# Optimization experiments

Measured on AMD Instinct MI355X. Metric: run time of the kernel, lower is better.

The kernel has to match this reference:

```python
import jax, jax.numpy as jnp
import numpy as np

SEQ, D, H, FF = 2048, 1024, 16, 4096
HD = D // H  # head_dim = 64


def setup_inputs() -> dict:
    key = jax.random.key(0)
    ks = jax.random.split(key, 13)
    s = lambda k, shape, fan_in: jax.random.normal(k, shape, jnp.float32) / np.sqrt(fan_in)
    return {
        "x":  jax.random.normal(ks[0], (SEQ, D), jnp.float32),
        # per-head Q/K/V linears, batched over the head axis: [H, D, HD]
        "Wq": s(ks[1], (H, D, HD), D), "bq": jnp.zeros((H, HD), jnp.float32),
        "Wk": s(ks[2], (H, D, HD), D), "bk": jnp.zeros((H, HD), jnp.float32),
        "Wv": s(ks[3], (H, D, HD), D), "bv": jnp.zeros((H, HD), jnp.float32),
        "Wp": s(ks[4], (D, D), D),     "bp": jnp.zeros((D,), jnp.float32),
        "W1": s(ks[5], (D, FF), D),    "b1": jnp.zeros((FF,), jnp.float32),
        "W2": s(ks[6], (FF, D), FF),   "b2": jnp.zeros((D,), jnp.float32),
    }


def reference(x, Wq, bq, Wk, bk, Wv, bv, Wp, bp, W1, b1, W2, b2):
    # Batched per-head projections: [H, S, HD]
    Qx = jnp.einsum("sd,hde->hse", x, Wq) + bq[:, None, :]
    Kx = jnp.einsum("sd,hde->hse", x, Wk) + bk[:, None, :]
    Vx = jnp.einsum("sd,hde->hse", x, Wv) + bv[:, None, :]
    # scores[h,s,t] = Qx[h,s]. Kx[h,t] / sqrt(HD); softmax over t (last dim)
    scores = jnp.einsum("hse,hte->hst", Qx, Kx) / jnp.sqrt(jnp.float32(HD))
    attn = jax.nn.softmax(scores, axis=-1)
    # Faithful to source: head[t,e] = sum_s Vx[s,e] * attn[s,t]  (attn^T @ V)
    heads = jnp.einsum("hse,hst->hte", Vx, attn)  # [H, S, HD]
    # concat heads along feature dim (head-major order) -> [S, D]
    concat = jnp.transpose(heads, (1, 0, 2)).reshape(SEQ, H * HD)
    proj = concat @ Wp + bp
    hidden = jax.nn.relu(proj @ W1 + b1)
    out = hidden @ W2 + b2
    return out
```

## Files before the change

### kernel.cpp

```cpp
#include <hip/hip_runtime.h>
#include <math.h>

constexpr int S_  = 2048;
constexpr int D_  = 1024;
constexpr int H_  = 16;
constexpr int HD_ = 64;
constexpr int FF_ = 4096;

typedef short bf16x8 __attribute__((ext_vector_type(8)));
typedef float f32x4  __attribute__((ext_vector_type(4)));

static __device__ __forceinline__ ushort f2bf(float f) {
    unsigned x = __float_as_uint(f);
    unsigned r = (x + 0x7fffu + ((x >> 16) & 1u)) >> 16;
    return (ushort)r;
}

static __device__ __forceinline__ void gload_lds16(const void* g, void* l) {
    __builtin_amdgcn_global_load_lds(
        (const __attribute__((address_space(1))) unsigned int*)g,
        (__attribute__((address_space(3))) unsigned int*)l, 16, 0, 0);
}

__global__ __launch_bounds__(256) void cast_f32_bf16(
    const float* __restrict__ in, ushort* __restrict__ out, int n)
{
    int i = (blockIdx.x * 256 + threadIdx.x) * 4;
    if (i < n) {
        float4 v = *(const float4*)(in + i);
        ushort4 o;
        o.x = f2bf(v.x); o.y = f2bf(v.y); o.z = f2bf(v.z); o.w = f2bf(v.w);
        *(ushort4*)(out + i) = o;
    }
}

__global__ __launch_bounds__(256) void transpose_cast(
    const float* __restrict__ in, ushort* __restrict__ out,
    int K, int N, long inZ, long outZ)
{
    const float* B = in + (size_t)blockIdx.z * inZ;
    ushort* BT = out + (size_t)blockIdx.z * outZ;
    __shared__ float Ts[32][33];
    const int n0 = blockIdx.x * 32, k0 = blockIdx.y * 32;
    const int r = threadIdx.x >> 3, c4 = (threadIdx.x & 7) * 4;
    float4 v = *(const float4*)(B + (size_t)(k0 + r) * N + n0 + c4);
    Ts[r][c4 + 0] = v.x; Ts[r][c4 + 1] = v.y;
    Ts[r][c4 + 2] = v.z; Ts[r][c4 + 3] = v.w;
    __syncthreads();
    ushort4 o;
    o.x = f2bf(Ts[c4 + 0][r]); o.y = f2bf(Ts[c4 + 1][r]);
    o.z = f2bf(Ts[c4 + 2][r]); o.w = f2bf(Ts[c4 + 3][r]);
    *(ushort4*)(BT + (size_t)(n0 + r) * K + k0 + c4) = o;
}

__global__ __launch_bounds__(256) void bias_cat(
    const float* __restrict__ bq, const float* __restrict__ bk,
    const float* __restrict__ bv, float* __restrict__ out)
{
    int i = blockIdx.x * 256 + threadIdx.x;
    float v = (i < 1024) ? bq[i] : (i < 2048 ? bk[i - 1024] : bv[i - 2048]);
    out[i] = v;
}

template <int BM, int BN, int WR, int WC, int KS, int RELU, int OUT>
__global__ __launch_bounds__(WR * WC * 64) void gemm_mfma(
    const ushort* __restrict__ A, const ushort* __restrict__ BT,
    const float* __restrict__ bias, void* __restrict__ Cv,
    int M, int N, int K)
{
    constexpr int WAVES = WR * WC;
    constexpr int WTM = BM / WR, WTN = BN / WC;
    constexpr int MT = WTM / 16, NT = WTN / 16;
    constexpr int AI = BM / 16;
    constexpr int TI = (BM + BN) / 16;
    constexpr int PW = TI / WAVES;

    __shared__ ushort As[BM * 32];
    __shared__ ushort Bs[BN * 32];

    const int tid = threadIdx.x;
    const int lane = tid & 63;
    const int wave = tid >> 6;
    const int wr = wave / WC, wc = wave % WC;
    const int row16 = lane & 15, kgrp = lane >> 4;
    const int m0 = blockIdx.y * BM, n0 = blockIdx.x * BN;
    const int kOff = blockIdx.z * (K / KS);

    const int lrow = lane >> 2;
    const int gcol8 = (lane & 3) ^ (lrow & 3);
    const int aslot = kgrp ^ (row16 & 3);

    f32x4 acc[MT][NT];
#pragma unroll
    for (int i = 0; i < MT; ++i)
#pragma unroll
        for (int j = 0; j < NT; ++j) acc[i][j] = (f32x4){0.f, 0.f, 0.f, 0.f};

    for (int k0 = kOff; k0 < kOff + K / KS; k0 += 32) {
        __syncthreads();
#pragma unroll
        for (int i = 0; i < PW; ++i) {
            const int inst = wave * PW + i;
            if (inst < AI) {
                const int row = inst * 16 + lrow;
                gload_lds16(A + (size_t)(m0 + row) * K + k0 + gcol8 * 8,
                            As + row * 32 + (lane & 3) * 8);
            } else {
                const int row = (inst - AI) * 16 + lrow;
                gload_lds16(BT + (size_t)(n0 + row) * K + k0 + gcol8 * 8,
                            Bs + row * 32 + (lane & 3) * 8);
            }
        }
        __syncthreads();

        bf16x8 af[MT], bfr[NT];
#pragma unroll
        for (int mt = 0; mt < MT; ++mt)
            af[mt] = *(const bf16x8*)(As + (wr * WTM + mt * 16 + row16) * 32 + aslot * 8);
#pragma unroll
        for (int nt = 0; nt < NT; ++nt)
            bfr[nt] = *(const bf16x8*)(Bs + (wc * WTN + nt * 16 + row16) * 32 + aslot * 8);
#pragma unroll
        for (int mt = 0; mt < MT; ++mt)
#pragma unroll
            for (int nt = 0; nt < NT; ++nt)
                acc[mt][nt] = __builtin_amdgcn_mfma_f32_16x16x32_bf16(
                    af[mt], bfr[nt], acc[mt][nt], 0, 0, 0);
    }

    if (OUT == 2) {
        float* Cp = (float*)Cv + (size_t)blockIdx.z * M * N;
#pragma unroll
        for (int nt = 0; nt < NT; ++nt) {
            const int n = n0 + wc * WTN + nt * 16 + row16;
#pragma unroll
            for (int mt = 0; mt < MT; ++mt)
#pragma unroll
                for (int r = 0; r < 4; ++r) {
                    const int m = m0 + wr * WTM + mt * 16 + kgrp * 4 + r;
                    Cp[(size_t)m * N + n] = acc[mt][nt][r];
                }
        }
    } else {
#pragma unroll
        for (int nt = 0; nt < NT; ++nt) {
            const int n = n0 + wc * WTN + nt * 16 + row16;
            const float bb = bias ? bias[n] : 0.f;
#pragma unroll
            for (int mt = 0; mt < MT; ++mt)
#pragma unroll
                for (int r = 0; r < 4; ++r) {
                    const int m = m0 + wr * WTM + mt * 16 + kgrp * 4 + r;
                    float v = acc[mt][nt][r] + bb;
                    if (RELU) v = fmaxf(v, 0.f);
                    if (OUT == 1)
                        ((ushort*)Cv)[(size_t)m * N + n] = f2bf(v);
                    else
                        ((float*)Cv)[(size_t)m * N + n] = v;
                }
        }
    }
}

__global__ __launch_bounds__(256) void reduce4_bias(
    const float* __restrict__ part, const float* __restrict__ bias,
    float* __restrict__ out, int MN, int N)
{
    const int i = (blockIdx.x * 256 + threadIdx.x) * 4;
    float4 a = *(const float4*)(part + i);
    const float4 b = *(const float4*)(part + (size_t)MN + i);
    const float4 c = *(const float4*)(part + 2 * (size_t)MN + i);
    const float4 d = *(const float4*)(part + 3 * (size_t)MN + i);
    const float4 e = *(const float4*)(bias + (i & (N - 1)));
    a.x += b.x + c.x + d.x + e.x;
    a.y += b.y + c.y + d.y + e.y;
    a.z += b.z + c.z + d.z + e.z;
    a.w += b.w + c.w + d.w + e.w;
    *(float4*)(out + i) = a;
}

__global__ __launch_bounds__(256) void attn_stats(
    const ushort* __restrict__ QKV, float* __restrict__ invL)
{
    const int h = blockIdx.y;
    const int s0 = blockIdx.x * 64;
    const int tid = threadIdx.x;
    const int lane = tid & 63;
    const int wave = tid >> 6;
    const int row16 = lane & 15;
    const int kgrp = lane >> 4;

    __shared__ ushort Ks[64 * 72];

    const ushort* Qrow = QKV + (size_t)(s0 + wave * 16 + row16) * 3072 + h * 64;
    bf16x8 qf0 = *(const bf16x8*)(Qrow + kgrp * 8);
    bf16x8 qf1 = *(const bf16x8*)(Qrow + kgrp * 8 + 32);

    float suml[4] = {0.f, 0.f, 0.f, 0.f};
    const int r0 = tid >> 3, c0 = (tid & 7) * 8;
    const ushort* Kbase = QKV + 1024 + h * 64;

    for (int t0 = 0; t0 < S_; t0 += 64) {
        uint4 ka = *(const uint4*)(Kbase + (size_t)(t0 + r0) * 3072 + c0);
        uint4 kb = *(const uint4*)(Kbase + (size_t)(t0 + 32 + r0) * 3072 + c0);
        __syncthreads();
        *(uint4*)(Ks + r0 * 72 + c0) = ka;
        *(uint4*)(Ks + (r0 + 32) * 72 + c0) = kb;
        __syncthreads();
#pragma unroll
        for (int nt = 0; nt < 4; ++nt) {
            f32x4 sc = (f32x4){0.f, 0.f, 0.f, 0.f};
            bf16x8 kf0 = *(const bf16x8*)(Ks + (nt * 16 + row16) * 72 + kgrp * 8);
            bf16x8 kf1 = *(const bf16x8*)(Ks + (nt * 16 + row16) * 72 + kgrp * 8 + 32);
            sc = __builtin_amdgcn_mfma_f32_16x16x32_bf16(qf0, kf0, sc, 0, 0, 0);
            sc = __builtin_amdgcn_mfma_f32_16x16x32_bf16(qf1, kf1, sc, 0, 0, 0);
#pragma unroll
            for (int r = 0; r < 4; ++r)
                suml[r] += __expf(sc[r] * 0.125f);
        }
    }
#pragma unroll
    for (int r = 0; r < 4; ++r) {
#pragma unroll
        for (int m = 1; m < 16; m <<= 1)
            suml[r] += __shfl_xor(suml[r], m, 64);
    }
    if (row16 == 0) {
#pragma unroll
        for (int r = 0; r < 4; ++r)
            invL[(size_t)h * S_ + s0 + wave * 16 + kgrp * 4 + r] = 1.f / suml[r];
    }
}

__global__ __launch_bounds__(256) void attn_pv(
    const ushort* __restrict__ QKV, const float* __restrict__ invL,
    ushort* __restrict__ concat)
{
    const int h = blockIdx.y;
    const int t0g = blockIdx.x * 64;
    const int tid = threadIdx.x;
    const int lane = tid & 63;
    const int wave = tid >> 6;
    const int row16 = lane & 15;
    const int kgrp = lane >> 4;

    __shared__ ushort Ks[64 * 72];
    __shared__ ushort Qs[64 * 72];
    __shared__ ushort VT[64 * 72];
    __shared__ ushort PT[64 * 72];

    const int r0 = tid >> 3, c0 = (tid & 7) * 8;

    {
        uint4 a = *(const uint4*)(QKV + (size_t)(t0g + r0) * 3072 + 1024 + h * 64 + c0);
        uint4 b = *(const uint4*)(QKV + (size_t)(t0g + 32 + r0) * 3072 + 1024 + h * 64 + c0);
        *(uint4*)(Ks + r0 * 72 + c0) = a;
        *(uint4*)(Ks + (r0 + 32) * 72 + c0) = b;
    }

    f32x4 oacc[4];
#pragma unroll
    for (int nt = 0; nt < 4; ++nt) oacc[nt] = (f32x4){0.f, 0.f, 0.f, 0.f};

    for (int s0 = 0; s0 < S_; s0 += 64) {
        uint4 qa = *(const uint4*)(QKV + (size_t)(s0 + r0) * 3072 + h * 64 + c0);
        uint4 qb = *(const uint4*)(QKV + (size_t)(s0 + 32 + r0) * 3072 + h * 64 + c0);
        uint4 v0 = *(const uint4*)(QKV + (size_t)(s0 + lane) * 3072 + 2048 + h * 64 + wave * 8);
        uint4 v1 = *(const uint4*)(QKV + (size_t)(s0 + lane) * 3072 + 2048 + h * 64 + (wave + 4) * 8);
        __syncthreads();
        *(uint4*)(Qs + r0 * 72 + c0) = qa;
        *(uint4*)(Qs + (r0 + 32) * 72 + c0) = qb;
        {
            union { uint4 u; ushort s[8]; } c1, c2;
            c1.u = v0; c2.u = v1;
#pragma unroll
            for (int i = 0; i < 8; ++i) {
                VT[(wave * 8 + i) * 72 + lane] = c1.s[i];
                VT[((wave + 4) * 8 + i) * 72 + lane] = c2.s[i];
            }
        }
        __syncthreads();

        float il[4];
#pragma unroll
        for (int r = 0; r < 4; ++r)
            il[r] = invL[(size_t)h * S_ + s0 + wave * 16 + kgrp * 4 + r];
        bf16x8 qf0 = *(const bf16x8*)(Qs + (wave * 16 + row16) * 72 + kgrp * 8);
        bf16x8 qf1 = *(const bf16x8*)(Qs + (wave * 16 + row16) * 72 + kgrp * 8 + 32);
#pragma unroll
        for (int nt = 0; nt < 4; ++nt) {
            f32x4 sc = (f32x4){0.f, 0.f, 0.f, 0.f};
            bf16x8 kf0 = *(const bf16x8*)(Ks + (nt * 16 + row16) * 72 + kgrp * 8);
            bf16x8 kf1 = *(const bf16x8*)(Ks + (nt * 16 + row16) * 72 + kgrp * 8 + 32);
            sc = __builtin_amdgcn_mfma_f32_16x16x32_bf16(qf0, kf0, sc, 0, 0, 0);
            sc = __builtin_amdgcn_mfma_f32_16x16x32_bf16(qf1, kf1, sc, 0, 0, 0);
#pragma unroll
            for (int r = 0; r < 4; ++r) {
                float p = __expf(sc[r] * 0.125f) * il[r];
                PT[(nt * 16 + row16) * 72 + wave * 16 + kgrp * 4 + r] = f2bf(p);
            }
        }
        __syncthreads();

        bf16x8 pf0 = *(const bf16x8*)(PT + (wave * 16 + row16) * 72 + kgrp * 8);
        bf16x8 pf1 = *(const bf16x8*)(PT + (wave * 16 + row16) * 72 + kgrp * 8 + 32);
#pragma unroll
        for (int nt = 0; nt < 4; ++nt) {
            bf16x8 vf0 = *(const bf16x8*)(VT + (nt * 16 + row16) * 72 + kgrp * 8);
            bf16x8 vf1 = *(const bf16x8*)(VT + (nt * 16 + row16) * 72 + kgrp * 8 + 32);
            oacc[nt] = __builtin_amdgcn_mfma_f32_16x16x32_bf16(pf0, vf0, oacc[nt], 0, 0, 0);
            oacc[nt] = __builtin_amdgcn_mfma_f32_16x16x32_bf16(pf1, vf1, oacc[nt], 0, 0, 0);
        }
    }

#pragma unroll
    for (int nt = 0; nt < 4; ++nt)
#pragma unroll
        for (int r = 0; r < 4; ++r) {
            const int t = t0g + wave * 16 + kgrp * 4 + r;
            const int e = nt * 16 + row16;
            concat[(size_t)t * D_ + h * HD_ + e] = f2bf(oacc[nt][r]);
        }
}

extern "C" void kernel_launch(void* const* d_in, const int* in_sizes, int n_in,
                              void* d_out, int out_size, void* d_ws,
                              size_t ws_size, hipStream_t stream)
{
    const float* x  = (const float*)d_in[0];
    const float* Wq = (const float*)d_in[1];
    const float* bq = (const float*)d_in[2];
    const float* Wk = (const float*)d_in[3];
    const float* bk = (const float*)d_in[4];
    const float* Wv = (const float*)d_in[5];
    const float* bv = (const float*)d_in[6];
    const float* Wp = (const float*)d_in[7];
    const float* bp = (const float*)d_in[8];
    const float* W1 = (const float*)d_in[9];
    const float* b1 = (const float*)d_in[10];
    const float* W2 = (const float*)d_in[11];
    const float* b2 = (const float*)d_in[12];
    float* out = (float*)d_out;

    constexpr size_t MB = 1u << 20;
    char* base = (char*)d_ws;
    ushort* xb      = (ushort*)(base +  0 * MB);
    ushort* BTqkv   = (ushort*)(base +  4 * MB);
    ushort* BTp     = (ushort*)(base + 10 * MB);
    ushort* BT1     = (ushort*)(base + 12 * MB);
    ushort* QKVcat  = (ushort*)(base + 20 * MB);
    ushort* concat  = (ushort*)(base + 32 * MB);
    ushort* projb   = (ushort*)(base + 36 * MB);
    float*  partial = (float*) (base +  0 * MB);
    ushort* BT2     = (ushort*)(base + 40 * MB);
    ushort* hidden  = (ushort*)(base + 48 * MB);
    float*  biascat = (float*) (base + 64 * MB);
    float*  invL    = biascat + 3072;

    cast_f32_bf16<<<dim3(S_ * D_ / 1024), 256, 0, stream>>>(x, xb, S_ * D_);
    transpose_cast<<<dim3(HD_ / 32, D_ / 32, H_), 256, 0, stream>>>(
        Wq, BTqkv,               D_, HD_, (long)D_ * HD_, (long)HD_ * D_);
    transpose_cast<<<dim3(HD_ / 32, D_ / 32, H_), 256, 0, stream>>>(
        Wk, BTqkv + 1024 * 1024, D_, HD_, (long)D_ * HD_, (long)HD_ * D_);
    transpose_cast<<<dim3(HD_ / 32, D_ / 32, H_), 256, 0, stream>>>(
        Wv, BTqkv + 2048 * 1024, D_, HD_, (long)D_ * HD_, (long)HD_ * D_);
    transpose_cast<<<dim3(D_ / 32, D_ / 32, 1), 256, 0, stream>>>(
        Wp, BTp, D_, D_, 0, 0);
    transpose_cast<<<dim3(FF_ / 32, D_ / 32, 1), 256, 0, stream>>>(
        W1, BT1, D_, FF_, 0, 0);
    transpose_cast<<<dim3(D_ / 32, FF_ / 32, 1), 256, 0, stream>>>(
        W2, BT2, FF_, D_, 0, 0);
    bias_cat<<<dim3(12), 256, 0, stream>>>(bq, bk, bv, biascat);

    gemm_mfma<128, 128, 2, 2, 1, 0, 1>
        <<<dim3(3072 / 128, S_ / 128, 1), 256, 0, stream>>>(
            xb, BTqkv, biascat, QKVcat, S_, 3072, D_);

    attn_stats<<<dim3(S_ / 64, H_), 256, 0, stream>>>(QKVcat, invL);
    attn_pv<<<dim3(S_ / 64, H_), 256, 0, stream>>>(QKVcat, invL, concat);

    gemm_mfma<64, 128, 1, 4, 1, 0, 1>
        <<<dim3(D_ / 128, S_ / 64, 1), 256, 0, stream>>>(
            concat, BTp, bp, projb, S_, D_, D_);

    gemm_mfma<128, 128, 2, 2, 1, 1, 1>
        <<<dim3(FF_ / 128, S_ / 128, 1), 256, 0, stream>>>(
            projb, BT1, b1, hidden, S_, FF_, D_);
    gemm_mfma<128, 128, 2, 2, 4, 0, 2>
        <<<dim3(D_ / 128, S_ / 128, 4), 256, 0, stream>>>(
            hidden, BT2, nullptr, partial, S_, D_, FF_);
    reduce4_bias<<<dim3(S_ * D_ / 1024), 256, 0, stream>>>(
        partial, b2, out, S_ * D_, D_);
}
```

Baseline: 323.6 us.

## Restructure attention: pre-scale transposed V, split over key chunks, swizzled LDS

```diff
diff --git a/kernel.cpp b/kernel.cpp
--- a/kernel.cpp
+++ b/kernel.cpp
@@ -14,6 +14,9 @@
     unsigned x = __float_as_uint(f);
     unsigned r = (x + 0x7fffu + ((x >> 16) & 1u)) >> 16;
     return (ushort)r;
+}
+static __device__ __forceinline__ float bf2f(ushort u) {
+    return __uint_as_float(((unsigned)u) << 16);
 }
 
 static __device__ __forceinline__ void gload_lds16(const void* g, void* l) {
@@ -66,7 +69,7 @@
 __global__ __launch_bounds__(WR * WC * 64) void gemm_mfma(
     const ushort* __restrict__ A, const ushort* __restrict__ BT,
     const float* __restrict__ bias, void* __restrict__ Cv,
-    int M, int N, int K)
+    void* __restrict__ Cv2, int M, int N, int K)
 {
     constexpr int WAVES = WR * WC;
     constexpr int WTM = BM / WR, WTN = BN / WC;
@@ -128,8 +131,9 @@
                     af[mt], bfr[nt], acc[mt][nt], 0, 0, 0);
     }
 
-    if (OUT == 2) {
-        float* Cp = (float*)Cv + (size_t)blockIdx.z * M * N;
+    if constexpr (OUT == 2) {
+        float* Cp = ((blockIdx.z < KS / 2) ? (float*)Cv : (float*)Cv2)
+                    + (size_t)(blockIdx.z % (KS / 2)) * M * N;
 #pragma unroll
         for (int nt = 0; nt < NT; ++nt) {
             const int n = n0 + wc * WTN + nt * 16 + row16;
@@ -140,6 +144,39 @@
                     const int m = m0 + wr * WTM + mt * 16 + kgrp * 4 + r;
                     Cp[(size_t)m * N + n] = acc[mt][nt][r];
                 }
+        }
+    } else if constexpr (OUT == 3) {
+        ushort* QKo = (ushort*)Cv;
+        ushort* VTo = (ushort*)Cv2;
+        if (n0 < 2048) {
+#pragma unroll
+            for (int nt = 0; nt < NT; ++nt) {
+                const int n = n0 + wc * WTN + nt * 16 + row16;
+                const float bb = bias[n];
+#pragma unroll
+                for (int mt = 0; mt < MT; ++mt)
+#pragma unroll
+                    for (int r = 0; r < 4; ++r) {
+                        const int m = m0 + wr * WTM + mt * 16 + kgrp * 4 + r;
+                        QKo[(size_t)m * 2048 + n] = f2bf(acc[mt][nt][r] + bb);
+                    }
+            }
+        } else {
+#pragma unroll
+            for (int nt = 0; nt < NT; ++nt) {
+                const int n = n0 + wc * WTN + nt * 16 + row16;
+                const float bb = bias[n];
+#pragma unroll
+                for (int mt = 0; mt < MT; ++mt) {
+                    const int mb = m0 + wr * WTM + mt * 16 + kgrp * 4;
+                    ushort4 o;
+                    o.x = f2bf(acc[mt][nt][0] + bb);
+                    o.y = f2bf(acc[mt][nt][1] + bb);
+                    o.z = f2bf(acc[mt][nt][2] + bb);
+                    o.w = f2bf(acc[mt][nt][3] + bb);
+                    *(ushort4*)(VTo + (size_t)(n - 2048) * 2048 + mb) = o;
+                }
+            }
         }
     } else {
 #pragma unroll
@@ -163,14 +200,14 @@
 }
 
 __global__ __launch_bounds__(256) void reduce4_bias(
-    const float* __restrict__ part, const float* __restrict__ bias,
-    float* __restrict__ out, int MN, int N)
+    const float* __restrict__ pA, const float* __restrict__ pB,
+    const float* __restrict__ bias, float* __restrict__ out, int MN, int N)
 {
     const int i = (blockIdx.x * 256 + threadIdx.x) * 4;
-    float4 a = *(const float4*)(part + i);
-    const float4 b = *(const float4*)(part + (size_t)MN + i);
-    const float4 c = *(const float4*)(part + 2 * (size_t)MN + i);
-    const float4 d = *(const float4*)(part + 3 * (size_t)MN + i);
+    float4 a = *(const float4*)(pA + i);
+    const float4 b = *(const float4*)(pA + (size_t)MN + i);
+    const float4 c = *(const float4*)(pB + i);
+    const float4 d = *(const float4*)(pB + (size_t)MN + i);
     const float4 e = *(const float4*)(bias + (i & (N - 1)));
     a.x += b.x + c.x + d.x + e.x;
     a.y += b.y + c.y + d.y + e.y;
@@ -180,147 +217,223 @@
 }
 
 __global__ __launch_bounds__(256) void attn_stats(
-    const ushort* __restrict__ QKV, float* __restrict__ invL)
+    const ushort* __restrict__ QK, float* __restrict__ part)
 {
     const int h = blockIdx.y;
-    const int s0 = blockIdx.x * 64;
+    const int s0 = blockIdx.x * 128;
+    const int tz = blockIdx.z;
     const int tid = threadIdx.x;
     const int lane = tid & 63;
-    const int wave = tid >> 6;
+    const int w = tid >> 6;
     const int row16 = lane & 15;
     const int kgrp = lane >> 4;
 
-    __shared__ ushort Ks[64 * 72];
-
-    const ushort* Qrow = QKV + (size_t)(s0 + wave * 16 + row16) * 3072 + h * 64;
-    bf16x8 qf0 = *(const bf16x8*)(Qrow + kgrp * 8);
-    bf16x8 qf1 = *(const bf16x8*)(Qrow + kgrp * 8 + 32);
-
-    float suml[4] = {0.f, 0.f, 0.f, 0.f};
-    const int r0 = tid >> 3, c0 = (tid & 7) * 8;
-    const ushort* Kbase = QKV + 1024 + h * 64;
-
-    for (int t0 = 0; t0 < S_; t0 += 64) {
-        uint4 ka = *(const uint4*)(Kbase + (size_t)(t0 + r0) * 3072 + c0);
-        uint4 kb = *(const uint4*)(Kbase + (size_t)(t0 + 32 + r0) * 3072 + c0);
-        __syncthreads();
-        *(uint4*)(Ks + r0 * 72 + c0) = ka;
-        *(uint4*)(Ks + (r0 + 32) * 72 + c0) = kb;
+    __shared__ ushort Ks[64 * 64];
+
+    bf16x8 qf[2][2];
+#pragma unroll
+    for (int mt = 0; mt < 2; ++mt) {
+        const ushort* qp = QK + (size_t)(s0 + w * 32 + mt * 16 + row16) * 2048 + h * 64;
+        qf[mt][0] = *(const bf16x8*)(qp + kgrp * 8);
+        qf[mt][1] = *(const bf16x8*)(qp + kgrp * 8 + 32);
+    }
+
+    float suml[2][4] = {{0.f}};
+    const int r0 = tid >> 3, c0 = tid & 7;
+    const int sl = (c0 ^ (r0 & 7)) * 8;
+
+    for (int ti = 0; ti < 8; ++ti) {
+        const int t0 = tz * 512 + ti * 64;
+        uint4 ka = *(const uint4*)(QK + (size_t)(t0 + r0) * 2048 + 1024 + h * 64 + c0 * 8);
+        uint4 kb = *(const uint4*)(QK + (size_t)(t0 + 32 + r0) * 2048 + 1024 + h * 64 + c0 * 8);
+        __syncthreads();
+        *(uint4*)(Ks + r0 * 64 + sl) = ka;
+        *(uint4*)(Ks + (r0 + 32) * 64 + sl) = kb;
         __syncthreads();
 #pragma unroll
         for (int nt = 0; nt < 4; ++nt) {
-            f32x4 sc = (f32x4){0.f, 0.f, 0.f, 0.f};
-            bf16x8 kf0 = *(const bf16x8*)(Ks + (nt * 16 + row16) * 72 + kgrp * 8);
-            bf16x8 kf1 = *(const bf16x8*)(Ks + (nt * 16 + row16) * 72 + kgrp * 8 + 32);
-            sc = __builtin_amdgcn_mfma_f32_16x16x32_bf16(qf0, kf0, sc, 0, 0, 0);
-            sc = __builtin_amdgcn_mfma_f32_16x16x32_bf16(qf1, kf1, sc, 0, 0, 0);
+            const int kr = nt * 16 + row16;
+            bf16x8 kf0 = *(const bf16x8*)(Ks + kr * 64 + ((kgrp ^ (kr & 7)) * 8));
+            bf16x8 kf1 = *(const bf16x8*)(Ks + kr * 64 + (((kgrp + 4) ^ (kr & 7)) * 8));
+#pragma unroll
+            for (int mt = 0; mt < 2; ++mt) {
+                f32x4 sc = (f32x4){0.f, 0.f, 0.f, 0.f};
+                sc = __builtin_amdgcn_mfma_f32_16x16x32_bf16(qf[mt][0], kf0, sc, 0, 0, 0);
+                sc = __builtin_amdgcn_mfma_f32_16x16x32_bf16(qf[mt][1], kf1, sc, 0, 0, 0);
+#pragma unroll
+                for (int r = 0; r < 4; ++r)
+                    suml[mt][r] += __expf(sc[r] * 0.125f);
+            }
+        }
+    }
+#pragma unroll
+    for (int mt = 0; mt < 2; ++mt)
+#pragma unroll
+        for (int r = 0; r < 4; ++r) {
+#pragma unroll
+            for (int m = 1; m < 16; m <<= 1)
+                suml[mt][r] += __shfl_xor(suml[mt][r], m, 64);
+        }
+    if (row16 == 0) {
+#pragma unroll
+        for (int mt = 0; mt < 2; ++mt)
 #pragma unroll
             for (int r = 0; r < 4; ++r)
-                suml[r] += __expf(sc[r] * 0.125f);
-        }
-    }
-#pragma unroll
-    for (int r = 0; r < 4; ++r) {
-#pragma unroll
-        for (int m = 1; m < 16; m <<= 1)
-            suml[r] += __shfl_xor(suml[r], m, 64);
-    }
-    if (row16 == 0) {
-#pragma unroll
-        for (int r = 0; r < 4; ++r)
-            invL[(size_t)h * S_ + s0 + wave * 16 + kgrp * 4 + r] = 1.f / suml[r];
-    }
+                part[((size_t)tz * H_ + h) * S_ + s0 + w * 32 + mt * 16 + kgrp * 4 + r]
+                    = suml[mt][r];
+    }
+}
+
+__global__ __launch_bounds__(256) void make_invL(
+    const float* __restrict__ part, float* __restrict__ invL)
+{
+    const int i = blockIdx.x * 256 + threadIdx.x;
+    const int HS = H_ * S_;
+    float s = part[i] + part[HS + i] + part[2 * HS + i] + part[3 * HS + i];
+    invL[i] = 1.f / s;
+}
+
+__global__ __launch_bounds__(256) void vscale(
+    ushort* __restrict__ VT, const float* __restrict__ invL)
+{
+    const int r = blockIdx.x;
+    const int c = threadIdx.x * 8;
+    const float* il = invL + (r >> 6) * S_ + c;
+    union { uint4 u; ushort s[8]; } v;
+    v.u = *(const uint4*)(VT + (size_t)r * S_ + c);
+    float4 l0 = *(const float4*)(il);
+    float4 l1 = *(const float4*)(il + 4);
+    v.s[0] = f2bf(bf2f(v.s[0]) * l0.x);
+    v.s[1] = f2bf(bf2f(v.s[1]) * l0.y);
+    v.s[2] = f2bf(bf2f(v.s[2]) * l0.z);
+    v.s[3] = f2bf(bf2f(v.s[3]) * l0.w);
+    v.s[4] = f2bf(bf2f(v.s[4]) * l1.x);
+    v.s[5] = f2bf(bf2f(v.s[5]) * l1.y);
+    v.s[6] = f2bf(bf2f(v.s[6]) * l1.z);
+    v.s[7] = f2bf(bf2f(v.s[7]) * l1.w);
+    *(uint4*)(VT + (size_t)r * S_ + c) = v.u;
 }
 
 __global__ __launch_bounds__(256) void attn_pv(
-    const ushort* __restrict__ QKV, const float* __restrict__ invL,
-    ushort* __restrict__ concat)
+    const ushort* __restrict__ QK, const ushort* __restrict__ VT,
+    ushort* __restrict__ pvp)
 {
     const int h = blockIdx.y;
-    const int t0g = blockIdx.x * 64;
+    const int t0 = blockIdx.x * 128;
+    const int sbase = blockIdx.z * 512;
     const int tid = threadIdx.x;
     const int lane = tid & 63;
-    const int wave = tid >> 6;
+    const int w = tid >> 6;
     const int row16 = lane & 15;
     const int kgrp = lane >> 4;
 
-    __shared__ ushort Ks[64 * 72];
-    __shared__ ushort Qs[64 * 72];
-    __shared__ ushort VT[64 * 72];
-    __shared__ ushort PT[64 * 72];
-
-    const int r0 = tid >> 3, c0 = (tid & 7) * 8;
-
-    {
-        uint4 a = *(const uint4*)(QKV + (size_t)(t0g + r0) * 3072 + 1024 + h * 64 + c0);
-        uint4 b = *(const uint4*)(QKV + (size_t)(t0g + 32 + r0) * 3072 + 1024 + h * 64 + c0);
-        *(uint4*)(Ks + r0 * 72 + c0) = a;
-        *(uint4*)(Ks + (r0 + 32) * 72 + c0) = b;
-    }
-
-    f32x4 oacc[4];
-#pragma unroll
-    for (int nt = 0; nt < 4; ++nt) oacc[nt] = (f32x4){0.f, 0.f, 0.f, 0.f};
-
-    for (int s0 = 0; s0 < S_; s0 += 64) {
-        uint4 qa = *(const uint4*)(QKV + (size_t)(s0 + r0) * 3072 + h * 64 + c0);
-        uint4 qb = *(const uint4*)(QKV + (size_t)(s0 + 32 + r0) * 3072 + h * 64 + c0);
-        uint4 v0 = *(const uint4*)(QKV + (size_t)(s0 + lane) * 3072 + 2048 + h * 64 + wave * 8);
-        uint4 v1 = *(const uint4*)(QKV + (size_t)(s0 + lane) * 3072 + 2048 + h * 64 + (wave + 4) * 8);
-        __syncthreads();
-        *(uint4*)(Qs + r0 * 72 + c0) = qa;
-        *(uint4*)(Qs + (r0 + 32) * 72 + c0) = qb;
-        {
-            union { uint4 u; ushort s[8]; } c1, c2;
-            c1.u = v0; c2.u = v1;
-#pragma unroll
-            for (int i = 0; i < 8; ++i) {
-                VT[(wave * 8 + i) * 72 + lane] = c1.s[i];
-                VT[((wave + 4) * 8 + i) * 72 + lane] = c2.s[i];
+    __shared__ ushort KP[128 * 64];
+    __shared__ ushort Qs[64 * 64];
+    __shared__ ushort Vs[64 * 64];
+
+    const int r0 = tid >> 3, c0 = tid & 7;
+    const int sl = (c0 ^ (r0 & 7)) * 8;
+
+#pragma unroll
+    for (int i = 0; i < 4; ++i) {
+        const int r = r0 + i * 32;
+        uint4 kv = *(const uint4*)(QK + (size_t)(t0 + r) * 2048 + 1024 + h * 64 + c0 * 8);
+        *(uint4*)(KP + r * 64 + sl) = kv;
+    }
+    __syncthreads();
+    bf16x8 kf[8][2];
+#pragma unroll
+    for (int nt = 0; nt < 8; ++nt) {
+        const int r = nt * 16 + row16;
+        kf[nt][0] = *(const bf16x8*)(KP + r * 64 + ((kgrp ^ (r & 7)) * 8));
+        kf[nt][1] = *(const bf16x8*)(KP + r * 64 + (((kgrp + 4) ^ (r & 7)) * 8));
+    }
+
+    f32x4 acc[2][4];
+#pragma unroll
+    for (int i = 0; i < 2; ++i)
+#pragma unroll
+        for (int j = 0; j < 4; ++j) acc[i][j] = (f32x4){0.f, 0.f, 0.f, 0.f};
+
+    for (int si = 0; si < 8; ++si) {
+        const int s0 = sbase + si * 64;
+        uint4 qa = *(const uint4*)(QK + (size_t)(s0 + r0) * 2048 + h * 64 + c0 * 8);
+        uint4 qb = *(const uint4*)(QK + (size_t)(s0 + 32 + r0) * 2048 + h * 64 + c0 * 8);
+        uint4 va = *(const uint4*)(VT + (size_t)(h * 64 + r0) * 2048 + s0 + c0 * 8);
+        uint4 vb = *(const uint4*)(VT + (size_t)(h * 64 + 32 + r0) * 2048 + s0 + c0 * 8);
+        __syncthreads();
+        *(uint4*)(Qs + r0 * 64 + sl) = qa;
+        *(uint4*)(Qs + (r0 + 32) * 64 + sl) = qb;
+        *(uint4*)(Vs + r0 * 64 + sl) = va;
+        *(uint4*)(Vs + (r0 + 32) * 64 + sl) = vb;
+        __syncthreads();
+
+        const int qr = w * 16 + row16;
+        bf16x8 qf0 = *(const bf16x8*)(Qs + qr * 64 + ((kgrp ^ (qr & 7)) * 8));
+        bf16x8 qf1 = *(const bf16x8*)(Qs + qr * 64 + (((kgrp + 4) ^ (qr & 7)) * 8));
+#pragma unroll
+        for (int nt = 0; nt < 8; ++nt) {
+            f32x4 sc = (f32x4){0.f, 0.f, 0.f, 0.f};
+            sc = __builtin_amdgcn_mfma_f32_16x16x32_bf16(qf0, kf[nt][0], sc, 0, 0, 0);
+            sc = __builtin_amdgcn_mfma_f32_16x16x32_bf16(qf1, kf[nt][1], sc, 0, 0, 0);
+            ushort4 o;
+            o.x = f2bf(__expf(sc[0] * 0.125f));
+            o.y = f2bf(__expf(sc[1] * 0.125f));
+            o.z = f2bf(__expf(sc[2] * 0.125f));
+            o.w = f2bf(__expf(sc[3] * 0.125f));
+            const int tl = nt * 16 + row16;
+            const int chunk = w * 2 + (kgrp >> 1);
+            *(ushort4*)(KP + tl * 64 + ((chunk ^ (tl & 7)) * 8) + (kgrp & 1) * 4) = o;
+        }
+        __syncthreads();
+
+        bf16x8 vf[4][2];
+#pragma unroll
+        for (int nt = 0; nt < 4; ++nt) {
+            const int vr = nt * 16 + row16;
+            vf[nt][0] = *(const bf16x8*)(Vs + vr * 64 + ((kgrp ^ (vr & 7)) * 8));
+            vf[nt][1] = *(const bf16x8*)(Vs + vr * 64 + (((kgrp + 4) ^ (vr & 7)) * 8));
+        }
+#pragma unroll
+        for (int mt = 0; mt < 2; ++mt) {
+            const int pr = w * 32 + mt * 16 + row16;
+            bf16x8 pf0 = *(const bf16x8*)(KP + pr * 64 + ((kgrp ^ (pr & 7)) * 8));
+            bf16x8 pf1 = *(const bf16x8*)(KP + pr * 64 + (((kgrp + 4) ^ (pr & 7)) * 8));
+#pragma unroll
+            for (int nt = 0; nt < 4; ++nt) {
+                acc[mt][nt] = __builtin_amdgcn_mfma_f32_16x16x32_bf16(pf0, vf[nt][0], acc[mt][nt], 0, 0, 0);
+                acc[mt][nt] = __builtin_amdgcn_mfma_f32_16x16x32_bf16(pf1, vf[nt][1], acc[mt][nt], 0, 0, 0);
             }
         }
-        __syncthreads();
-
-        float il[4];
-#pragma unroll
-        for (int r = 0; r < 4; ++r)
-            il[r] = invL[(size_t)h * S_ + s0 + wave * 16 + kgrp * 4 + r];
-        bf16x8 qf0 = *(const bf16x8*)(Qs + (wave * 16 + row16) * 72 + kgrp * 8);
-        bf16x8 qf1 = *(const bf16x8*)(Qs + (wave * 16 + row16) * 72 + kgrp * 8 + 32);
-#pragma unroll
-        for (int nt = 0; nt < 4; ++nt) {
-            f32x4 sc = (f32x4){0.f, 0.f, 0.f, 0.f};
-            bf16x8 kf0 = *(const bf16x8*)(Ks + (nt * 16 + row16) * 72 + kgrp * 8);
-            bf16x8 kf1 = *(const bf16x8*)(Ks + (nt * 16 + row16) * 72 + kgrp * 8 + 32);
-            sc = __builtin_amdgcn_mfma_f32_16x16x32_bf16(qf0, kf0, sc, 0, 0, 0);
-            sc = __builtin_amdgcn_mfma_f32_16x16x32_bf16(qf1, kf1, sc, 0, 0, 0);
+    }
+
+    ushort* dst = pvp + (size_t)blockIdx.z * S_ * D_;
+#pragma unroll
+    for (int mt = 0; mt < 2; ++mt)
+#pragma unroll
+        for (int nt = 0; nt < 4; ++nt)
 #pragma unroll
             for (int r = 0; r < 4; ++r) {
-                float p = __expf(sc[r] * 0.125f) * il[r];
-                PT[(nt * 16 + row16) * 72 + wave * 16 + kgrp * 4 + r] = f2bf(p);
+                const int t = t0 + w * 32 + mt * 16 + kgrp * 4 + r;
+                const int e = nt * 16 + row16;
+                dst[(size_t)t * D_ + h * 64 + e] = f2bf(acc[mt][nt][r]);
             }
-        }
-        __syncthreads();
-
-        bf16x8 pf0 = *(const bf16x8*)(PT + (wave * 16 + row16) * 72 + kgrp * 8);
-        bf16x8 pf1 = *(const bf16x8*)(PT + (wave * 16 + row16) * 72 + kgrp * 8 + 32);
-#pragma unroll
-        for (int nt = 0; nt < 4; ++nt) {
-            bf16x8 vf0 = *(const bf16x8*)(VT + (nt * 16 + row16) * 72 + kgrp * 8);
-            bf16x8 vf1 = *(const bf16x8*)(VT + (nt * 16 + row16) * 72 + kgrp * 8 + 32);
-            oacc[nt] = __builtin_amdgcn_mfma_f32_16x16x32_bf16(pf0, vf0, oacc[nt], 0, 0, 0);
-            oacc[nt] = __builtin_amdgcn_mfma_f32_16x16x32_bf16(pf1, vf1, oacc[nt], 0, 0, 0);
-        }
-    }
-
-#pragma unroll
-    for (int nt = 0; nt < 4; ++nt)
-#pragma unroll
-        for (int r = 0; r < 4; ++r) {
-            const int t = t0g + wave * 16 + kgrp * 4 + r;
-            const int e = nt * 16 + row16;
-            concat[(size_t)t * D_ + h * HD_ + e] = f2bf(oacc[nt][r]);
-        }
+}
+
+__global__ __launch_bounds__(256) void reduce_cat(
+    const ushort* __restrict__ p, ushort* __restrict__ concat)
+{
+    const size_t SD = (size_t)S_ * D_;
+    const size_t i = ((size_t)blockIdx.x * 256 + threadIdx.x) * 8;
+    union { uint4 u; ushort s[8]; } a, b, c, d, o;
+    a.u = *(const uint4*)(p + i);
+    b.u = *(const uint4*)(p + SD + i);
+    c.u = *(const uint4*)(p + 2 * SD + i);
+    d.u = *(const uint4*)(p + 3 * SD + i);
+#pragma unroll
+    for (int j = 0; j < 8; ++j)
+        o.s[j] = f2bf(bf2f(a.s[j]) + bf2f(b.s[j]) + bf2f(c.s[j]) + bf2f(d.s[j]));
+    *(uint4*)(concat + i) = o.u;
 }
 
 extern "C" void kernel_launch(void* const* d_in, const int* in_sizes, int n_in,
@@ -344,18 +457,22 @@
 
     constexpr size_t MB = 1u << 20;
     char* base = (char*)d_ws;
-    ushort* xb      = (ushort*)(base +  0 * MB);
-    ushort* BTqkv   = (ushort*)(base +  4 * MB);
-    ushort* BTp     = (ushort*)(base + 10 * MB);
-    ushort* BT1     = (ushort*)(base + 12 * MB);
-    ushort* QKVcat  = (ushort*)(base + 20 * MB);
-    ushort* concat  = (ushort*)(base + 32 * MB);
-    ushort* projb   = (ushort*)(base + 36 * MB);
-    float*  partial = (float*) (base +  0 * MB);
-    ushort* BT2     = (ushort*)(base + 40 * MB);
-    ushort* hidden  = (ushort*)(base + 48 * MB);
-    float*  biascat = (float*) (base + 64 * MB);
-    float*  invL    = biascat + 3072;
+    ushort* BT2    = (ushort*)(base +  0 * MB);
+    ushort* BT1    = (ushort*)(base +  8 * MB);
+    ushort* BTp    = (ushort*)(base + 16 * MB);
+    ushort* xb     = (ushort*)(base + 18 * MB);
+    ushort* concat = (ushort*)(base + 18 * MB);
+    ushort* BTqkv  = (ushort*)(base + 22 * MB);
+    ushort* projb  = (ushort*)(base + 22 * MB);
+    ushort* QKcat  = (ushort*)(base + 28 * MB);
+    ushort* hidden = (ushort*)(base + 28 * MB);
+    ushort* VTg    = (ushort*)(base + 36 * MB);
+    ushort* pvp    = (ushort*)(base + 40 * MB);
+    float*  ff2a   = (float*) (base +  8 * MB);
+    float*  ff2b   = (float*) (base + 44 * MB);
+    float*  biascat= (float*) (base + 60 * MB);
+    float*  invL   = biascat + 3072;
+    float*  statsP = invL + H_ * S_;
 
     cast_f32_bf16<<<dim3(S_ * D_ / 1024), 256, 0, stream>>>(x, xb, S_ * D_);
     transpose_cast<<<dim3(HD_ / 32, D_ / 32, H_), 256, 0, stream>>>(
@@ -372,23 +489,31 @@
         W2, BT2, FF_, D_, 0, 0);
     bias_cat<<<dim3(12), 256, 0, stream>>>(bq, bk, bv, biascat);
 
-    gemm_mfma<128, 128, 2, 2, 1, 0, 1>
+    gemm_mfma<128, 128, 2, 2, 1, 0, 3>
         <<<dim3(3072 / 128, S_ / 128, 1), 256, 0, stream>>>(
-            xb, BTqkv, biascat, QKVcat, S_, 3072, D_);
-
-    attn_stats<<<dim3(S_ / 64, H_), 256, 0, stream>>>(QKVcat, invL);
-    attn_pv<<<dim3(S_ / 64, H_), 256, 0, stream>>>(QKVcat, invL, concat);
+            xb, BTqkv, biascat, QKcat, VTg, S_, 3072, D_);
+
+    attn_stats<<<dim3(S_ / 128, H_, 4), 256, 0, stream>>>(QKcat, statsP);
+    make_invL<<<dim3(H_ * S_ / 256), 256, 0, stream>>>(statsP, invL);
+
+    vscale<<<dim3(D_), 256, 0, stream>>>(VTg, invL);
+
+    attn_pv<<<dim3(S_ / 128, H_, 4), 256, 0, stream>>>(QKcat, VTg, pvp);
+
+    reduce_cat<<<dim3(S_ * D_ / 2048), 256, 0, stream>>>(pvp, concat);
 
     gemm_mfma<64, 128, 1, 4, 1, 0, 1>
         <<<dim3(D_ / 128, S_ / 64, 1), 256, 0, stream>>>(
-            concat, BTp, bp, projb, S_, D_, D_);
+            concat, BTp, bp, projb, nullptr, S_, D_, D_);
 
     gemm_mfma<128, 128, 2, 2, 1, 1, 1>
         <<<dim3(FF_ / 128, S_ / 128, 1), 256, 0, stream>>>(
-            projb, BT1, b1, hidden, S_, FF_, D_);
+            projb, BT1, b1, hidden, nullptr, S_, FF_, D_);
+
     gemm_mfma<128, 128, 2, 2, 4, 0, 2>
         <<<dim3(D_ / 128, S_ / 128, 4), 256, 0, stream>>>(
-            hidden, BT2, nullptr, partial, S_, D_, FF_);
+            hidden, BT2, nullptr, ff2a, ff2b, S_, D_, FF_);
+
     reduce4_bias<<<dim3(S_ * D_ / 1024), 256, 0, stream>>>(
-        partial, b2, out, S_ * D_, D_);
-}
+        ff2a, ff2b, b2, out, S_ * D_, D_);
+}
```

Result: faster. 306.9 us (-5.1%).
